# Performance work log

Hardware: AMD Instinct MI355X
Metric: run time of the kernel (lower is better)

Reference implementation:

```python
import jax, jax.numpy as jnp
import numpy as np

B, S, H, NH = 1, 2048, 768, 12
HD = H // NH  # 64


def setup_inputs() -> dict:
    key = jax.random.key(0)
    k0, k1, k2, k3 = jax.random.split(key, 4)
    BN = B * S
    return {
        "hidden_states": jax.random.normal(k0, (B, S, H), dtype=jnp.float32),
        "g": jax.random.uniform(k1, (BN, BN), dtype=jnp.float32),
        "attention_mask": jnp.zeros((B, S), dtype=jnp.float32),
        "Wq": jax.random.normal(k2, (H, H), dtype=jnp.float32) * 0.02,
        "bq": jnp.zeros((H,), dtype=jnp.float32),
        "Wv": jax.random.normal(k3, (H, H), dtype=jnp.float32) * 0.02,
        "bv": jnp.zeros((H,), dtype=jnp.float32),
    }


def reference(hidden_states, g, attention_mask, Wq, bq, Wv, bv):
    # hidden_states: [B, S, H] -> torch code transposes to [S, B, H]
    hs = jnp.swapaxes(hidden_states, 0, 1)  # [S, B, H]
    s, b, h = hs.shape
    BN = s * b

    q = hs @ Wq.T + bq  # [S, B, H]
    v = hs @ Wv.T + bv  # [S, B, H]

    # view(S,B,NH,HD).transpose(0,1) -> [B,S,NH,HD], then flat reshape to [NH, BN, HD]
    q = jnp.swapaxes(q.reshape(s, b, NH, HD), 0, 1).reshape(NH, BN, HD)
    # L2-normalize each query vector along head_dim (torch F.normalize, eps=1e-12)
    q = q / jnp.maximum(jnp.linalg.norm(q, axis=2, keepdims=True), 1e-12)

    # value: [B,S,NH,HD] flattened to [BN, NH, HD]
    v = jnp.swapaxes(v.reshape(s, b, NH, HD), 0, 1).reshape(BN, NH, HD)

    # attn sparsification mask combine (computed in original, but never used downstream)
    bool_mask = (attention_mask >= 0).reshape(-1, 1).astype(g.dtype)  # [BN, 1]
    _g_masked = g * (bool_mask @ bool_mask.T)  # dead value, kept for faithfulness

    # L2-distance attention scores: -(AA - 2AB + BB) / sqrt(head_dim)
    AB = jnp.einsum('hnd,hmd->hnm', q, q)            # [NH, BN, BN]
    AA = jnp.sum(q * q, axis=-1, keepdims=True)      # [NH, BN, 1]
    sim = -(AA - 2.0 * AB + jnp.swapaxes(AA, -1, -2)) * (HD ** -0.5)
    attn = jax.nn.softmax(sim, axis=-1)              # [NH, BN, BN]

    # weighted value sum: bmm(attn, v.transpose(0,1)) -> [NH, BN, HD]
    out = jnp.einsum('hnm,hmd->hnd', attn, jnp.swapaxes(v, 0, 1))

    # reshape(B,S,NH,HD) then merge last two dims -> [B, S, H]
    out = out.reshape(b, s, NH, HD).reshape(b, s, h)
    return out
```

## Files before the change

### kernel.cpp

```cpp
#include <hip/hip_runtime.h>
#include <math.h>

#define NTOK 2048
#define HDIM 768
#define NHEAD 12
#define NVEC (NTOK * NHEAD)

typedef __attribute__((ext_vector_type(8))) short short8v;
typedef __attribute__((ext_vector_type(4))) float float4v;

static __device__ __forceinline__ unsigned short f2bf(float x) {
    unsigned u = __float_as_uint(x);
    return (unsigned short)((u + 0x7fffu + ((u >> 16) & 1u)) >> 16);
}

static __device__ __forceinline__ void gload_lds16(const void* g, void* lds_uniform) {
    __builtin_amdgcn_global_load_lds(
        (const __attribute__((address_space(1))) void*)g,
        (__attribute__((address_space(3))) void*)lds_uniform, 16, 0, 0);
}

__global__ __launch_bounds__(128) void proj_kernel(
    const float* __restrict__ hs, const float* __restrict__ Wq,
    const float* __restrict__ bq, const float* __restrict__ Wv,
    const float* __restrict__ bv, float* __restrict__ qout,
    unsigned short* __restrict__ vT)
{
    constexpr int PITCH = 40;
    __shared__ unsigned short As[2][64 * PITCH];
    __shared__ unsigned short Bs[2][64 * PITCH];

    const float* W    = blockIdx.z ? Wv : Wq;
    const float* bias = blockIdx.z ? bv : bq;
    const int n0 = blockIdx.x * 64, m0 = blockIdx.y * 64;
    const int tid = threadIdx.x, lane = tid & 63, w = tid >> 6;

    const int sr = tid >> 1, sc = (tid & 1) * 16;
    const float* agp = hs + (size_t)(m0 + sr) * HDIM + sc;
    const float* bgp = W  + (size_t)(n0 + sr) * HDIM + sc;

    float4 ga[4], gb[4];
    #pragma unroll
    for (int i = 0; i < 4; ++i) {
        ga[i] = *(const float4*)(agp + i * 4);
        gb[i] = *(const float4*)(bgp + i * 4);
    }

    float4v acc[2][4];
    #pragma unroll
    for (int rs = 0; rs < 2; ++rs)
        #pragma unroll
        for (int t = 0; t < 4; ++t) acc[rs][t] = (float4v){0.f, 0.f, 0.f, 0.f};

    for (int kk = 0; kk < 24; ++kk) {
        const int b = kk & 1;
        union { unsigned short u[16]; short8v v[2]; } pa, pb;
        #pragma unroll
        for (int i = 0; i < 4; ++i) {
            pa.u[i*4+0] = f2bf(ga[i].x); pa.u[i*4+1] = f2bf(ga[i].y);
            pa.u[i*4+2] = f2bf(ga[i].z); pa.u[i*4+3] = f2bf(ga[i].w);
            pb.u[i*4+0] = f2bf(gb[i].x); pb.u[i*4+1] = f2bf(gb[i].y);
            pb.u[i*4+2] = f2bf(gb[i].z); pb.u[i*4+3] = f2bf(gb[i].w);
        }
        *(short8v*)&As[b][sr * PITCH + sc]     = pa.v[0];
        *(short8v*)&As[b][sr * PITCH + sc + 8] = pa.v[1];
        *(short8v*)&Bs[b][sr * PITCH + sc]     = pb.v[0];
        *(short8v*)&Bs[b][sr * PITCH + sc + 8] = pb.v[1];

        if (kk < 23) {
            agp += 32; bgp += 32;
            #pragma unroll
            for (int i = 0; i < 4; ++i) {
                ga[i] = *(const float4*)(agp + i * 4);
                gb[i] = *(const float4*)(bgp + i * 4);
            }
        }
        __syncthreads();

        short8v af0 = *(const short8v*)&As[b][(w*32 +      (lane & 15)) * PITCH + ((lane >> 4) << 3)];
        short8v af1 = *(const short8v*)&As[b][(w*32 + 16 + (lane & 15)) * PITCH + ((lane >> 4) << 3)];
        #pragma unroll
        for (int t = 0; t < 4; ++t) {
            short8v bf = *(const short8v*)&Bs[b][((lane & 15) + 16*t) * PITCH + ((lane >> 4) << 3)];
            acc[0][t] = __builtin_amdgcn_mfma_f32_16x16x32_bf16(af0, bf, acc[0][t], 0, 0, 0);
            acc[1][t] = __builtin_amdgcn_mfma_f32_16x16x32_bf16(af1, bf, acc[1][t], 0, 0, 0);
        }
    }

    float bcol[4];
    #pragma unroll
    for (int t = 0; t < 4; ++t) bcol[t] = bias[n0 + (lane & 15) + 16*t];

    if (blockIdx.z == 0) {
        #pragma unroll
        for (int rs = 0; rs < 2; ++rs)
            #pragma unroll
            for (int t = 0; t < 4; ++t)
                #pragma unroll
                for (int r = 0; r < 4; ++r) {
                    int m = m0 + w*32 + rs*16 + ((lane >> 4) << 2) + r;
                    qout[(size_t)m * HDIM + n0 + (lane & 15) + 16*t] = acc[rs][t][r] + bcol[t];
                }
    } else {
        #pragma unroll
        for (int rs = 0; rs < 2; ++rs)
            #pragma unroll
            for (int t = 0; t < 4; ++t) {
                int f = n0 + (lane & 15) + 16*t;
                int mb = m0 + w*32 + rs*16 + ((lane >> 4) << 2);
                union { unsigned short u[4]; unsigned long long q; } pk;
                #pragma unroll
                for (int r = 0; r < 4; ++r) pk.u[r] = f2bf(acc[rs][t][r] + bcol[t]);
                *(unsigned long long*)(vT + (size_t)f * NTOK + mb) = pk.q;
            }
    }
}

__global__ __launch_bounds__(256) void norm_kernel(const float* __restrict__ q,
                                                   unsigned short* __restrict__ qbf)
{
    int gid  = blockIdx.x * 256 + threadIdx.x;
    int vi   = gid >> 6;
    int lane = threadIdx.x & 63;
    float x  = q[(size_t)vi * 64 + lane];
    float ss = x * x;
    #pragma unroll
    for (int m = 1; m < 64; m <<= 1) ss += __shfl_xor(ss, m);
    float inv = 1.0f / fmaxf(sqrtf(ss), 1e-12f);
    qbf[(size_t)vi * 64 + lane] = f2bf(x * inv);
}

__global__ __launch_bounds__(128) void attn_kernel(
    const unsigned short* __restrict__ qbf,
    const unsigned short* __restrict__ vT,
    float* __restrict__ out)
{
    __shared__ unsigned short Ksb[2][64 * 64];
    __shared__ unsigned short Vsb[2][64 * 64];
    __shared__ unsigned short Psb[2][16 * 64];

    const int bid = blockIdx.x;
    const int swz = (bid & 7) * 96 + (bid >> 3);
    const int h = swz >> 6, n0 = (swz & 63) * 32;
    const int tid = threadIdx.x, lane = tid & 63, w = tid >> 6;

    const unsigned short* qrow =
        qbf + ((size_t)h * NTOK + n0 + w * 16 + (lane & 15)) * 64;
    short8v qa[2];
    qa[0] = *(const short8v*)(qrow + ((lane >> 4) << 3));
    qa[1] = *(const short8v*)(qrow + 32 + ((lane >> 4) << 3));

    const unsigned short* kh = qbf + (size_t)h * NTOK * 64;
    const unsigned short* vh = vT + (size_t)h * 64 * NTOK;

#define STAGE(buf, m0v)                                                        \
    {                                                                          \
        const unsigned short* kbase = kh + (size_t)(m0v) * 64;                 \
        const unsigned short* vbase = vh + (m0v);                              \
        _Pragma("unroll")                                                      \
        for (int i = 0; i < 4; ++i) {                                          \
            int ci = ((w * 4 + i) << 6) + lane;                                \
            int r = ci >> 3, c8 = ci & 7;                                      \
            int cs = (c8 ^ (r & 7)) << 3;                                      \
            gload_lds16(kbase + (r << 6) + cs,                                 \
                        (char*)&Ksb[buf][0] + ((w * 4 + i) << 10));            \
            gload_lds16(vbase + r * NTOK + cs,                                 \
                        (char*)&Vsb[buf][0] + ((w * 4 + i) << 10));            \
        }                                                                      \
    }

    float4v acc[4];
    #pragma unroll
    for (int t = 0; t < 4; ++t) acc[t] = (float4v){0.f, 0.f, 0.f, 0.f};
    float lsum[4] = {0.f, 0.f, 0.f, 0.f};

    STAGE(0, 0);
    __syncthreads();
    int cur = 0;

    for (int mt = 0; mt < 32; ++mt) {
        if (mt < 31) STAGE(cur ^ 1, (mt + 1) * 64);

        float4v S[4];
        #pragma unroll
        for (int t = 0; t < 4; ++t) {
            S[t] = (float4v){0.f, 0.f, 0.f, 0.f};
            #pragma unroll
            for (int kk = 0; kk < 2; ++kk) {
                int row = (lane & 15) + (t << 4);
                int off = ((row << 7) + (kk << 6) + ((lane >> 4) << 4)) ^ ((row & 7) << 4);
                short8v kf = *(const short8v*)((const char*)&Ksb[cur][0] + off);
                S[t] = __builtin_amdgcn_mfma_f32_16x16x32_bf16(qa[kk], kf, S[t], 0, 0, 0);
            }
        }

        float p[4][4];
        #pragma unroll
        for (int t = 0; t < 4; ++t)
            #pragma unroll
            for (int r = 0; r < 4; ++r)
                p[t][r] = __expf(S[t][r] * 0.25f);

        #pragma unroll
        for (int r = 0; r < 4; ++r) {
            float ss = p[0][r] + p[1][r] + p[2][r] + p[3][r];
            ss += __shfl_xor(ss, 1);
            ss += __shfl_xor(ss, 2);
            ss += __shfl_xor(ss, 4);
            ss += __shfl_xor(ss, 8);
            lsum[r] += ss;
        }

        #pragma unroll
        for (int t = 0; t < 4; ++t)
            #pragma unroll
            for (int r = 0; r < 4; ++r) {
                int pr = ((lane >> 4) << 2) + r, pc = (lane & 15) + (t << 4);
                int off = ((pr << 7) + (pc << 1)) ^ ((pr & 7) << 4);
                *(unsigned short*)((char*)&Psb[w][0] + off) = f2bf(p[t][r]);
            }

        #pragma unroll
        for (int kk = 0; kk < 2; ++kk) {
            int prr = lane & 15;
            int poff = ((prr << 7) + (kk << 6) + ((lane >> 4) << 4)) ^ ((prr & 7) << 4);
            short8v pf = *(const short8v*)((const char*)&Psb[w][0] + poff);
            #pragma unroll
            for (int t = 0; t < 4; ++t) {
                int vr = (lane & 15) + (t << 4);
                int voff = ((vr << 7) + (kk << 6) + ((lane >> 4) << 4)) ^ ((vr & 7) << 4);
                short8v vf = *(const short8v*)((const char*)&Vsb[cur][0] + voff);
                acc[t] = __builtin_amdgcn_mfma_f32_16x16x32_bf16(pf, vf, acc[t], 0, 0, 0);
            }
        }

        __syncthreads();
        cur ^= 1;
    }
#undef STAGE

    float inv[4];
    #pragma unroll
    for (int r = 0; r < 4; ++r) inv[r] = 1.0f / lsum[r];
    #pragma unroll
    for (int t = 0; t < 4; ++t)
        #pragma unroll
        for (int r = 0; r < 4; ++r) {
            int n = n0 + w * 16 + ((lane >> 4) << 2) + r;
            int d = (lane & 15) + (t << 4);
            out[((size_t)h * NTOK + n) * 64 + d] = acc[t][r] * inv[r];
        }
}

extern "C" void kernel_launch(void* const* d_in, const int* in_sizes, int n_in,
                              void* d_out, int out_size, void* d_ws, size_t ws_size,
                              hipStream_t stream)
{
    const float* hs = (const float*)d_in[0];
    const float* Wq = (const float*)d_in[3];
    const float* bq = (const float*)d_in[4];
    const float* Wv = (const float*)d_in[5];
    const float* bv = (const float*)d_in[6];
    float* out = (float*)d_out;

    float*          q_full = (float*)d_ws;
    unsigned short* qbf    = (unsigned short*)(q_full + (size_t)NTOK * HDIM);
    unsigned short* vT     = qbf + (size_t)NVEC * 64;

    proj_kernel<<<dim3(HDIM / 64, NTOK / 64, 2), 128, 0, stream>>>(
        hs, Wq, bq, Wv, bv, q_full, vT);
    norm_kernel<<<dim3(NVEC * 64 / 256), 256, 0, stream>>>(q_full, qbf);
    attn_kernel<<<dim3(768), 128, 0, stream>>>(qbf, vT, out);
}
```

Baseline: 156.4 us.

## Precast inputs to bf16, fuse q-normalize into projection, register-stream K/V in attention

Adds a separate cast kernel that converts hidden states and both weight matrices to bf16 up front. The projection GEMM then uses async global-to-LDS loads with larger 128x64 tiles and 256 threads, and it fuses the L2 normalization of q into its epilogue, so the norm kernel and the fp32 q round-trip go away. The attention kernel drops LDS staging of K and V and loads MFMA fragments straight from global memory into registers, prefetching the next tile. It also uses s_setprio, packed bf16 conversion and a simpler row-sum reduction. The changes trade an extra launch and extra global traffic for the cast against less LDS and sync overhead, and rely on the cache to serve the repeated K/V reads.

Measured after the change: 182.4 us. +16.6%, slower.

```diff
diff --git a/kernel.cpp b/kernel.cpp
--- a/kernel.cpp
+++ b/kernel.cpp
@@ -4,7 +4,6 @@
 #define NTOK 2048
 #define HDIM 768
 #define NHEAD 12
-#define NVEC (NTOK * NHEAD)
 
 typedef __attribute__((ext_vector_type(8))) short short8v;
 typedef __attribute__((ext_vector_type(4))) float float4v;
@@ -20,114 +19,134 @@
         (__attribute__((address_space(3))) void*)lds_uniform, 16, 0, 0);
 }
 
-__global__ __launch_bounds__(128) void proj_kernel(
+__global__ __launch_bounds__(256) void cast_kernel(
     const float* __restrict__ hs, const float* __restrict__ Wq,
-    const float* __restrict__ bq, const float* __restrict__ Wv,
-    const float* __restrict__ bv, float* __restrict__ qout,
+    const float* __restrict__ Wv, unsigned short* __restrict__ hsb,
+    unsigned short* __restrict__ wqb, unsigned short* __restrict__ wvb)
+{
+    int gid = blockIdx.x * 256 + threadIdx.x;
+    const float* src; unsigned short* dst; int off;
+    if (gid < 393216)      { src = hs; dst = hsb; off = gid; }
+    else if (gid < 540672) { src = Wq; dst = wqb; off = gid - 393216; }
+    else                   { src = Wv; dst = wvb; off = gid - 540672; }
+    float4 v = ((const float4*)src)[off];
+    union { unsigned short u[4]; unsigned long long q; } pk;
+    pk.u[0] = f2bf(v.x); pk.u[1] = f2bf(v.y);
+    pk.u[2] = f2bf(v.z); pk.u[3] = f2bf(v.w);
+    *(unsigned long long*)(dst + (size_t)off * 4) = pk.q;
+}
+
+__global__ __launch_bounds__(256) void projnorm_kernel(
+    const unsigned short* __restrict__ hsb, const unsigned short* __restrict__ wqb,
+    const unsigned short* __restrict__ wvb, const float* __restrict__ bq,
+    const float* __restrict__ bv, unsigned short* __restrict__ qbf,
     unsigned short* __restrict__ vT)
 {
-    constexpr int PITCH = 40;
-    __shared__ unsigned short As[2][64 * PITCH];
-    __shared__ unsigned short Bs[2][64 * PITCH];
-
-    const float* W    = blockIdx.z ? Wv : Wq;
-    const float* bias = blockIdx.z ? bv : bq;
-    const int n0 = blockIdx.x * 64, m0 = blockIdx.y * 64;
+    __shared__ unsigned short Asb[2][128 * 64];
+    __shared__ unsigned short Bsb[2][64 * 64];
+
     const int tid = threadIdx.x, lane = tid & 63, w = tid >> 6;
-
-    const int sr = tid >> 1, sc = (tid & 1) * 16;
-    const float* agp = hs + (size_t)(m0 + sr) * HDIM + sc;
-    const float* bgp = W  + (size_t)(n0 + sr) * HDIM + sc;
-
-    float4 ga[4], gb[4];
-    #pragma unroll
-    for (int i = 0; i < 4; ++i) {
-        ga[i] = *(const float4*)(agp + i * 4);
-        gb[i] = *(const float4*)(bgp + i * 4);
+    const int m0 = blockIdx.y * 128;
+    const bool isq = (blockIdx.x < 12);
+    const int n0 = (blockIdx.x % 12) * 64;
+    const unsigned short* Wb = (isq ? wqb : wvb) + (size_t)n0 * HDIM;
+    const float* bias = isq ? bq : bv;
+
+#define STAGEP(buf, k0)                                                        \
+    {                                                                          \
+        _Pragma("unroll")                                                      \
+        for (int i = 0; i < 4; ++i) {                  \
+            int ci = ((w * 4 + i) << 6) + lane;                                \
+            int r = ci >> 3, c8 = (ci & 7) ^ (r & 7);                          \
+            gload_lds16(hsb + (size_t)(m0 + r) * HDIM + (k0) + (c8 << 3),      \
+                        (char*)&Asb[buf][0] + ((w * 4 + i) << 10));            \
+        }                                                                      \
+        _Pragma("unroll")                                                      \
+        for (int i = 0; i < 2; ++i) {                   \
+            int ci = ((w * 2 + i) << 6) + lane;                                \
+            int r = ci >> 3, c8 = (ci & 7) ^ (r & 7);                          \
+            gload_lds16(Wb + (size_t)r * HDIM + (k0) + (c8 << 3),              \
+                        (char*)&Bsb[buf][0] + ((w * 2 + i) << 10));            \
+        }                                                                      \
     }
 
     float4v acc[2][4];
     #pragma unroll
-    for (int rs = 0; rs < 2; ++rs)
-        #pragma unroll
-        for (int t = 0; t < 4; ++t) acc[rs][t] = (float4v){0.f, 0.f, 0.f, 0.f};
-
-    for (int kk = 0; kk < 24; ++kk) {
-        const int b = kk & 1;
-        union { unsigned short u[16]; short8v v[2]; } pa, pb;
-        #pragma unroll
-        for (int i = 0; i < 4; ++i) {
-            pa.u[i*4+0] = f2bf(ga[i].x); pa.u[i*4+1] = f2bf(ga[i].y);
-            pa.u[i*4+2] = f2bf(ga[i].z); pa.u[i*4+3] = f2bf(ga[i].w);
-            pb.u[i*4+0] = f2bf(gb[i].x); pb.u[i*4+1] = f2bf(gb[i].y);
-            pb.u[i*4+2] = f2bf(gb[i].z); pb.u[i*4+3] = f2bf(gb[i].w);
-        }
-        *(short8v*)&As[b][sr * PITCH + sc]     = pa.v[0];
-        *(short8v*)&As[b][sr * PITCH + sc + 8] = pa.v[1];
-        *(short8v*)&Bs[b][sr * PITCH + sc]     = pb.v[0];
-        *(short8v*)&Bs[b][sr * PITCH + sc + 8] = pb.v[1];
-
-        if (kk < 23) {
-            agp += 32; bgp += 32;
-            #pragma unroll
-            for (int i = 0; i < 4; ++i) {
-                ga[i] = *(const float4*)(agp + i * 4);
-                gb[i] = *(const float4*)(bgp + i * 4);
-            }
+    for (int fr = 0; fr < 2; ++fr)
+        #pragma unroll
+        for (int fc = 0; fc < 4; ++fc) acc[fr][fc] = (float4v){0.f, 0.f, 0.f, 0.f};
+
+    STAGEP(0, 0);
+    __syncthreads();
+
+    for (int ks = 0; ks < 12; ++ks) {
+        const int b = ks & 1;
+        if (ks < 11) STAGEP(b ^ 1, (ks + 1) * 64);
+        #pragma unroll
+        for (int kk = 0; kk < 2; ++kk) {
+            short8v af[2], bf[4];
+            #pragma unroll
+            for (int fr = 0; fr < 2; ++fr) {
+                int row = w * 32 + fr * 16 + (lane & 15);
+                int byt = ((row << 7) + (kk << 6) + ((lane >> 4) << 4)) ^ ((row & 7) << 4);
+                af[fr] = *(const short8v*)((const char*)&Asb[b][0] + byt);
+            }
+            #pragma unroll
+            for (int fc = 0; fc < 4; ++fc) {
+                int row = fc * 16 + (lane & 15);
+                int byt = ((row << 7) + (kk << 6) + ((lane >> 4) << 4)) ^ ((row & 7) << 4);
+                bf[fc] = *(const short8v*)((const char*)&Bsb[b][0] + byt);
+            }
+            #pragma unroll
+            for (int fr = 0; fr < 2; ++fr)
+                #pragma unroll
+                for (int fc = 0; fc < 4; ++fc)
+                    acc[fr][fc] = __builtin_amdgcn_mfma_f32_16x16x32_bf16(
+                        af[fr], bf[fc], acc[fr][fc], 0, 0, 0);
         }
         __syncthreads();
-
-        short8v af0 = *(const short8v*)&As[b][(w*32 +      (lane & 15)) * PITCH + ((lane >> 4) << 3)];
-        short8v af1 = *(const short8v*)&As[b][(w*32 + 16 + (lane & 15)) * PITCH + ((lane >> 4) << 3)];
-        #pragma unroll
-        for (int t = 0; t < 4; ++t) {
-            short8v bf = *(const short8v*)&Bs[b][((lane & 15) + 16*t) * PITCH + ((lane >> 4) << 3)];
-            acc[0][t] = __builtin_amdgcn_mfma_f32_16x16x32_bf16(af0, bf, acc[0][t], 0, 0, 0);
-            acc[1][t] = __builtin_amdgcn_mfma_f32_16x16x32_bf16(af1, bf, acc[1][t], 0, 0, 0);
-        }
-    }
+    }
+#undef STAGEP
 
     float bcol[4];
     #pragma unroll
-    for (int t = 0; t < 4; ++t) bcol[t] = bias[n0 + (lane & 15) + 16*t];
-
-    if (blockIdx.z == 0) {
-        #pragma unroll
-        for (int rs = 0; rs < 2; ++rs)
-            #pragma unroll
-            for (int t = 0; t < 4; ++t)
-                #pragma unroll
-                for (int r = 0; r < 4; ++r) {
-                    int m = m0 + w*32 + rs*16 + ((lane >> 4) << 2) + r;
-                    qout[(size_t)m * HDIM + n0 + (lane & 15) + 16*t] = acc[rs][t][r] + bcol[t];
+    for (int fc = 0; fc < 4; ++fc) bcol[fc] = bias[n0 + fc * 16 + (lane & 15)];
+
+    if (isq) {
+        #pragma unroll
+        for (int fr = 0; fr < 2; ++fr)
+            #pragma unroll
+            for (int r = 0; r < 4; ++r) {
+                float v[4];
+                float ss = 0.f;
+                #pragma unroll
+                for (int fc = 0; fc < 4; ++fc) {
+                    v[fc] = acc[fr][fc][r] + bcol[fc];
+                    ss = fmaf(v[fc], v[fc], ss);
                 }
+                ss += __shfl_xor(ss, 1);
+                ss += __shfl_xor(ss, 2);
+                ss += __shfl_xor(ss, 4);
+                ss += __shfl_xor(ss, 8);
+                float inv = 1.0f / fmaxf(sqrtf(ss), 1e-12f);
+                int m = m0 + w * 32 + fr * 16 + ((lane >> 4) << 2) + r;
+                #pragma unroll
+                for (int fc = 0; fc < 4; ++fc)
+                    qbf[(size_t)m * HDIM + n0 + fc * 16 + (lane & 15)] = f2bf(v[fc] * inv);
+            }
     } else {
         #pragma unroll
-        for (int rs = 0; rs < 2; ++rs)
-            #pragma unroll
-            for (int t = 0; t < 4; ++t) {
-                int f = n0 + (lane & 15) + 16*t;
-                int mb = m0 + w*32 + rs*16 + ((lane >> 4) << 2);
+        for (int fr = 0; fr < 2; ++fr)
+            #pragma unroll
+            for (int fc = 0; fc < 4; ++fc) {
+                int f = n0 + fc * 16 + (lane & 15);
+                int mtk = m0 + w * 32 + fr * 16 + ((lane >> 4) << 2);
                 union { unsigned short u[4]; unsigned long long q; } pk;
                 #pragma unroll
-                for (int r = 0; r < 4; ++r) pk.u[r] = f2bf(acc[rs][t][r] + bcol[t]);
-                *(unsigned long long*)(vT + (size_t)f * NTOK + mb) = pk.q;
-            }
-    }
-}
-
-__global__ __launch_bounds__(256) void norm_kernel(const float* __restrict__ q,
-                                                   unsigned short* __restrict__ qbf)
-{
-    int gid  = blockIdx.x * 256 + threadIdx.x;
-    int vi   = gid >> 6;
-    int lane = threadIdx.x & 63;
-    float x  = q[(size_t)vi * 64 + lane];
-    float ss = x * x;
-    #pragma unroll
-    for (int m = 1; m < 64; m <<= 1) ss += __shfl_xor(ss, m);
-    float inv = 1.0f / fmaxf(sqrtf(ss), 1e-12f);
-    qbf[(size_t)vi * 64 + lane] = f2bf(x * inv);
+                for (int r = 0; r < 4; ++r) pk.u[r] = f2bf(acc[fr][fc][r] + bcol[fc]);
+                *(unsigned long long*)(vT + (size_t)f * NTOK + mtk) = pk.q;
+            }
+    }
 }
 
 __global__ __launch_bounds__(128) void attn_kernel(
@@ -135,121 +154,117 @@
     const unsigned short* __restrict__ vT,
     float* __restrict__ out)
 {
-    __shared__ unsigned short Ksb[2][64 * 64];
-    __shared__ unsigned short Vsb[2][64 * 64];
-    __shared__ unsigned short Psb[2][16 * 64];
+    __shared__ unsigned short Pl[2][16 * 72];
 
     const int bid = blockIdx.x;
     const int swz = (bid & 7) * 96 + (bid >> 3);
-    const int h = swz >> 6, n0 = (swz & 63) * 32;
+    const int h = swz >> 6, qt = swz & 63;
     const int tid = threadIdx.x, lane = tid & 63, w = tid >> 6;
-
-    const unsigned short* qrow =
-        qbf + ((size_t)h * NTOK + n0 + w * 16 + (lane & 15)) * 64;
+    const int n0 = qt * 32 + w * 16;
+
+    const unsigned short* kh = qbf + (size_t)h * NTOK * 64;
+    const unsigned short* vh = vT + (size_t)h * 64 * NTOK;
+
+    const unsigned short* qrow = kh + ((size_t)n0 + (lane & 15)) * 64;
     short8v qa[2];
     qa[0] = *(const short8v*)(qrow + ((lane >> 4) << 3));
     qa[1] = *(const short8v*)(qrow + 32 + ((lane >> 4) << 3));
 
-    const unsigned short* kh = qbf + (size_t)h * NTOK * 64;
-    const unsigned short* vh = vT + (size_t)h * 64 * NTOK;
-
-#define STAGE(buf, m0v)                                                        \
-    {                                                                          \
-        const unsigned short* kbase = kh + (size_t)(m0v) * 64;                 \
-        const unsigned short* vbase = vh + (m0v);                              \
-        _Pragma("unroll")                                                      \
-        for (int i = 0; i < 4; ++i) {                                          \
-            int ci = ((w * 4 + i) << 6) + lane;                                \
-            int r = ci >> 3, c8 = ci & 7;                                      \
-            int cs = (c8 ^ (r & 7)) << 3;                                      \
-            gload_lds16(kbase + (r << 6) + cs,                                 \
-                        (char*)&Ksb[buf][0] + ((w * 4 + i) << 10));            \
-            gload_lds16(vbase + r * NTOK + cs,                                 \
-                        (char*)&Vsb[buf][0] + ((w * 4 + i) << 10));            \
-        }                                                                      \
-    }
+    short8v kf[8], vf[8];
+#define LOADK(mb)                                                              \
+    _Pragma("unroll")                                                          \
+    for (int t = 0; t < 4; ++t)                                                \
+        _Pragma("unroll")                                                      \
+        for (int kk = 0; kk < 2; ++kk)                                         \
+            kf[t * 2 + kk] = *(const short8v*)(                                \
+                kh + ((size_t)((mb) + t * 16 + (lane & 15))) * 64 +            \
+                kk * 32 + ((lane >> 4) << 3));
+#define LOADV(mb)                                                              \
+    _Pragma("unroll")                                                          \
+    for (int t = 0; t < 4; ++t)                                                \
+        _Pragma("unroll")                                                      \
+        for (int kk = 0; kk < 2; ++kk)                                         \
+            vf[t * 2 + kk] = *(const short8v*)(                                \
+                vh + (size_t)(t * 16 + (lane & 15)) * NTOK + (mb) +            \
+                kk * 32 + ((lane >> 4) << 3));
 
     float4v acc[4];
     #pragma unroll
     for (int t = 0; t < 4; ++t) acc[t] = (float4v){0.f, 0.f, 0.f, 0.f};
-    float lsum[4] = {0.f, 0.f, 0.f, 0.f};
-
-    STAGE(0, 0);
-    __syncthreads();
-    int cur = 0;
+    float lsum = 0.f;
+
+    LOADK(0);
+    LOADV(0);
 
     for (int mt = 0; mt < 32; ++mt) {
-        if (mt < 31) STAGE(cur ^ 1, (mt + 1) * 64);
-
-        float4v S[4];
+        float4v St[4];
+        __builtin_amdgcn_s_setprio(1);
         #pragma unroll
         for (int t = 0; t < 4; ++t) {
-            S[t] = (float4v){0.f, 0.f, 0.f, 0.f};
-            #pragma unroll
-            for (int kk = 0; kk < 2; ++kk) {
-                int row = (lane & 15) + (t << 4);
-                int off = ((row << 7) + (kk << 6) + ((lane >> 4) << 4)) ^ ((row & 7) << 4);
-                short8v kf = *(const short8v*)((const char*)&Ksb[cur][0] + off);
-                S[t] = __builtin_amdgcn_mfma_f32_16x16x32_bf16(qa[kk], kf, S[t], 0, 0, 0);
-            }
-        }
+            St[t] = (float4v){0.f, 0.f, 0.f, 0.f};
+            St[t] = __builtin_amdgcn_mfma_f32_16x16x32_bf16(kf[t*2+0], qa[0], St[t], 0, 0, 0);
+            St[t] = __builtin_amdgcn_mfma_f32_16x16x32_bf16(kf[t*2+1], qa[1], St[t], 0, 0, 0);
+        }
+        __builtin_amdgcn_s_setprio(0);
+
+        if (mt < 31) LOADK((mt + 1) * 64);
 
         float p[4][4];
+        float ls = 0.f;
         #pragma unroll
         for (int t = 0; t < 4; ++t)
             #pragma unroll
-            for (int r = 0; r < 4; ++r)
-                p[t][r] = __expf(S[t][r] * 0.25f);
-
-        #pragma unroll
-        for (int r = 0; r < 4; ++r) {
-            float ss = p[0][r] + p[1][r] + p[2][r] + p[3][r];
-            ss += __shfl_xor(ss, 1);
-            ss += __shfl_xor(ss, 2);
-            ss += __shfl_xor(ss, 4);
-            ss += __shfl_xor(ss, 8);
-            lsum[r] += ss;
-        }
-
+            for (int r = 0; r < 4; ++r) {
+                p[t][r] = __expf(St[t][r] * 0.25f);
+                ls += p[t][r];
+            }
+        ls += __shfl_xor(ls, 16);
+        ls += __shfl_xor(ls, 32);
+        lsum += ls;
+
+        #pragma unroll
+        for (int t = 0; t < 4; ++t) {
+            unsigned w0, w1;
+            asm volatile("v_cvt_pk_bf16_f32 %0, %1, %2"
+                         : "=v"(w0) : "v"(p[t][0]), "v"(p[t][1]));
+            asm volatile("v_cvt_pk_bf16_f32 %0, %1, %2"
+                         : "=v"(w1) : "v"(p[t][2]), "v"(p[t][3]));
+            unsigned long long q64 = (unsigned long long)w0 |
+                                     ((unsigned long long)w1 << 32);
+            *(unsigned long long*)(&Pl[w][(lane & 15) * 72 + t * 16 +
+                                          ((lane >> 4) << 2)]) = q64;
+        }
+        asm volatile("s_waitcnt lgkmcnt(0)" ::: "memory");
+        __builtin_amdgcn_sched_barrier(0);
+
+        short8v pf[2];
+        #pragma unroll
+        for (int kk = 0; kk < 2; ++kk)
+            pf[kk] = *(const short8v*)(&Pl[w][(lane & 15) * 72 + kk * 32 +
+                                              ((lane >> 4) << 3)]);
+
+        __builtin_amdgcn_s_setprio(1);
+        #pragma unroll
+        for (int t = 0; t < 4; ++t) {
+            acc[t] = __builtin_amdgcn_mfma_f32_16x16x32_bf16(pf[0], vf[t*2+0], acc[t], 0, 0, 0);
+            acc[t] = __builtin_amdgcn_mfma_f32_16x16x32_bf16(pf[1], vf[t*2+1], acc[t], 0, 0, 0);
+        }
+        __builtin_amdgcn_s_setprio(0);
+
+        if (mt < 31) LOADV((mt + 1) * 64);
+    }
+#undef LOADK
+#undef LOADV
+
+    #pragma unroll
+    for (int r = 0; r < 4; ++r) {
+        float lv = __shfl(lsum, ((lane >> 4) << 2) + r);
+        float inv = 1.0f / lv;
+        int n = n0 + ((lane >> 4) << 2) + r;
         #pragma unroll
         for (int t = 0; t < 4; ++t)
-            #pragma unroll
-            for (int r = 0; r < 4; ++r) {
-                int pr = ((lane >> 4) << 2) + r, pc = (lane & 15) + (t << 4);
-                int off = ((pr << 7) + (pc << 1)) ^ ((pr & 7) << 4);
-                *(unsigned short*)((char*)&Psb[w][0] + off) = f2bf(p[t][r]);
-            }
-
-        #pragma unroll
-        for (int kk = 0; kk < 2; ++kk) {
-            int prr = lane & 15;
-            int poff = ((prr << 7) + (kk << 6) + ((lane >> 4) << 4)) ^ ((prr & 7) << 4);
-            short8v pf = *(const short8v*)((const char*)&Psb[w][0] + poff);
-            #pragma unroll
-            for (int t = 0; t < 4; ++t) {
-                int vr = (lane & 15) + (t << 4);
-                int voff = ((vr << 7) + (kk << 6) + ((lane >> 4) << 4)) ^ ((vr & 7) << 4);
-                short8v vf = *(const short8v*)((const char*)&Vsb[cur][0] + voff);
-                acc[t] = __builtin_amdgcn_mfma_f32_16x16x32_bf16(pf, vf, acc[t], 0, 0, 0);
-            }
-        }
-
-        __syncthreads();
-        cur ^= 1;
-    }
-#undef STAGE
-
-    float inv[4];
-    #pragma unroll
-    for (int r = 0; r < 4; ++r) inv[r] = 1.0f / lsum[r];
-    #pragma unroll
-    for (int t = 0; t < 4; ++t)
-        #pragma unroll
-        for (int r = 0; r < 4; ++r) {
-            int n = n0 + w * 16 + ((lane >> 4) << 2) + r;
-            int d = (lane & 15) + (t << 4);
-            out[((size_t)h * NTOK + n) * 64 + d] = acc[t][r] * inv[r];
-        }
+            out[((size_t)h * NTOK + n) * 64 + t * 16 + (lane & 15)] = acc[t][r] * inv;
+    }
 }
 
 extern "C" void kernel_launch(void* const* d_in, const int* in_sizes, int n_in,
@@ -263,12 +278,13 @@
     const float* bv = (const float*)d_in[6];
     float* out = (float*)d_out;
 
-    float*          q_full = (float*)d_ws;
-    unsigned short* qbf    = (unsigned short*)(q_full + (size_t)NTOK * HDIM);
-    unsigned short* vT     = qbf + (size_t)NVEC * 64;
-
-    proj_kernel<<<dim3(HDIM / 64, NTOK / 64, 2), 128, 0, stream>>>(
-        hs, Wq, bq, Wv, bv, q_full, vT);
-    norm_kernel<<<dim3(NVEC * 64 / 256), 256, 0, stream>>>(q_full, qbf);
+    unsigned short* hsb = (unsigned short*)d_ws;
+    unsigned short* wqb = hsb + (size_t)NTOK * HDIM;
+    unsigned short* wvb = wqb + (size_t)HDIM * HDIM;
+    unsigned short* qbf = wvb + (size_t)HDIM * HDIM;
+    unsigned short* vT  = qbf + (size_t)NTOK * HDIM;
+
+    cast_kernel<<<dim3(2688), 256, 0, stream>>>(hs, Wq, Wv, hsb, wqb, wvb);
+    projnorm_kernel<<<dim3(24, 16), 256, 0, stream>>>(hsb, wqb, wvb, bq, bv, qbf, vT);
     attn_kernel<<<dim3(768), 128, 0, stream>>>(qbf, vT, out);
 }
```
